# Kernel tuning notes

Hardware: AMD Instinct MI355X
Metric: run time of the kernel (lower is better)

The kernel has to match this reference:

```python
import jax, jax.numpy as jnp
import numpy as np

BOX = 120          # box_size
RES = 1.0          # resolution (also Gaussian sigma)
NTYPES = 11        # num_atom_types (hard-coded in module)
D = 2              # splat half-width in cells -> (2D+1)^3 = 125 voxels/atom
B = 4
NATOMS = 2200      # 200 atoms per type


def setup_inputs() -> dict:
    key = jax.random.key(0)
    # atoms uniformly inside the box interior so splats mostly land in-bounds
    coords = jax.random.uniform(key, (B, NATOMS * 3), dtype=jnp.float32,
                                minval=20.0, maxval=100.0)
    per_type = NATOMS // NTYPES
    num_atoms_of_type = jnp.full((B, NTYPES), per_type, dtype=jnp.int32)
    offsets = jnp.tile(jnp.arange(NTYPES, dtype=jnp.int32) * per_type, (B, 1))
    return {"input_coords": coords,
            "num_atoms_of_type": num_atoms_of_type,
            "offsets": offsets}


def _splat(coords, num_atoms_of_type, offsets):
    # coords: [B, N, 3]; per-atom Gaussian splat into typed volume
    Bn, N, _ = coords.shape
    atom_idx = jnp.arange(N)

    def per_batch_types(off, num):
        # atoms [off[t], off[t]+num[t]) belong to type t
        t = jnp.clip(jnp.searchsorted(off, atom_idx, side='right') - 1, 0, NTYPES - 1)
        valid = (atom_idx >= off[t]) & (atom_idx < off[t] + num[t])
        return t, valid

    types, valid = jax.vmap(per_batch_types)(offsets, num_atoms_of_type)  # [B,N]

    # (2D+1)^3 window of integer cell offsets
    w = jnp.arange(-D, D + 1)
    wx, wy, wz = jnp.meshgrid(w, w, w, indexing='ij')
    win = jnp.stack([wx.ravel(), wy.ravel(), wz.ravel()], axis=-1)  # [W,3]

    base = jnp.floor(coords / RES).astype(jnp.int32)                 # [B,N,3]
    cells = base[:, :, None, :] + win[None, None, :, :]              # [B,N,W,3]
    centers = cells.astype(coords.dtype) * RES                       # voxel coords
    r2 = jnp.sum((centers - coords[:, :, None, :]) ** 2, axis=-1)    # [B,N,W]
    vals = jnp.exp(-r2 / (RES * RES))                                # Gaussian density

    inb = jnp.all((cells >= 0) & (cells < BOX), axis=-1)             # [B,N,W]
    ok = inb & valid[:, :, None]
    flat = (types[:, :, None] * (BOX * BOX * BOX)
            + cells[..., 0] * (BOX * BOX) + cells[..., 1] * BOX + cells[..., 2])
    flat = jnp.where(ok, flat, NTYPES * BOX * BOX * BOX)  # out-of-range -> dropped
    vals = jnp.where(ok, vals, jnp.zeros_like(vals))

    def scatter(f, v):
        vol = jnp.zeros((NTYPES * BOX * BOX * BOX,), dtype=coords.dtype)
        return vol.at[f.ravel()].add(v.ravel(), mode='drop')

    vol = jax.vmap(scatter)(flat, vals)
    return vol.reshape(Bn, NTYPES, BOX, BOX, BOX)


def reference(input_coords, num_atoms_of_type, offsets):
    coords = input_coords.reshape(input_coords.shape[0], -1, 3)
    return _splat(coords, num_atoms_of_type, offsets)
```

## Files before the change

### kernel.cpp

```cpp
#include <hip/hip_runtime.h>


#define BOX    120
#define NTYPES 11
#define DHALF  2
#define BOX3   (BOX * BOX * BOX)

#define BINSZ   4
#define NBIN    30
#define NBIN2   (NBIN * NBIN)
#define CAP     64

__global__ void zero_counts_kernel(int* __restrict__ counts, int n) {
    int i = blockIdx.x * blockDim.x + threadIdx.x;
    if (i < n) counts[i] = 0;
}

__global__ void bin_kernel(const float* __restrict__ coords,
                           const int*  __restrict__ num_atoms_of_type,
                           const int*  __restrict__ offsets,
                           float4* __restrict__ bins,
                           int*    __restrict__ counts,
                           int batch, int natoms) {
    int gid = blockIdx.x * blockDim.x + threadIdx.x;
    if (gid >= batch * natoms) return;
    int b = gid / natoms;
    int i = gid - b * natoms;

    const float* c = coords + ((long long)b * natoms + i) * 3;
    float x = c[0], y = c[1], z = c[2];

    const int* off = offsets           + b * NTYPES;
    const int* num = num_atoms_of_type + b * NTYPES;

    int t = 0;
#pragma unroll
    for (int k = 1; k < NTYPES; ++k)
        if (off[k] <= i) t = k;
    if (!(i >= off[t] && i < off[t] + num[t])) return;

    int bx = (int)floorf(x);
    int by = (int)floorf(y);
    int bz = (int)floorf(z);
    if (bx < -DHALF || bx >= BOX + DHALF ||
        by < -DHALF || by >= BOX + DHALF ||
        bz < -DHALF || bz >= BOX + DHALF) return;

    int cbx = min(BOX - 1, max(0, bx)) / BINSZ;
    int cby = min(BOX - 1, max(0, by)) / BINSZ;
    int bin = b * NBIN2 + cbx * NBIN + cby;

    int slot = atomicAdd(&counts[bin], 1);
    if (slot < CAP)
        bins[(long long)bin * CAP + slot] =
            make_float4(x, y, z, __int_as_float(t));
}

__global__ void gather_kernel(const float4* __restrict__ bins,
                              const int*    __restrict__ counts,
                              float* __restrict__ out) {
    int bid = blockIdx.x;
    int y = bid % BOX; bid /= BOX;
    int x = bid % BOX; bid /= BOX;
    int b = bid;
    int z = threadIdx.x;
    bool zon = (z < BOX);

    float acc[NTYPES];
#pragma unroll
    for (int k = 0; k < NTYPES; ++k) acc[k] = 0.f;

    int bx0 = max(0, x - DHALF) / BINSZ;
    int bx1 = min(BOX - 1, x + DHALF) / BINSZ;
    int by0 = max(0, y - DHALF) / BINSZ;
    int by1 = min(BOX - 1, y + DHALF) / BINSZ;

    for (int cbx = bx0; cbx <= bx1; ++cbx) {
        for (int cby = by0; cby <= by1; ++cby) {
            int bin = b * NBIN2 + cbx * NBIN + cby;
            int cnt = min(counts[bin], CAP);
            const float4* lst = bins + (long long)bin * CAP;
            for (int j = 0; j < cnt; ++j) {
                float4 a = lst[j];
                int abx = (int)floorf(a.x);
                int aby = (int)floorf(a.y);
                int abz = (int)floorf(a.z);
                if (abs(x - abx) > DHALF || abs(y - aby) > DHALF) continue;
                bool hit = zon && (abs(z - abz) <= DHALF);
                float dx = (float)x - a.x;
                float dy = (float)y - a.y;
                float dz = (float)z - a.z;
                float r2 = dx * dx + dy * dy + dz * dz;
                float val = hit ? expf(-r2) : 0.f;
                int t = __float_as_int(a.w);
#pragma unroll
                for (int k = 0; k < NTYPES; ++k)
                    acc[k] += (t == k) ? val : 0.f;
            }
        }
    }

    if (zon) {
        int base = x * (BOX * BOX) + y * BOX + z;
#pragma unroll
        for (int k = 0; k < NTYPES; ++k)
            out[(long long)(b * NTYPES + k) * BOX3 + base] = acc[k];
    }
}

extern "C" void kernel_launch(void* const* d_in, const int* in_sizes, int n_in,
                              void* d_out, int out_size, void* d_ws, size_t ws_size,
                              hipStream_t stream) {
    const float* coords = (const float*)d_in[0];
    const int*   num    = (const int*)d_in[1];
    const int*   off    = (const int*)d_in[2];
    float*       out    = (float*)d_out;

    int batch  = in_sizes[1] / NTYPES;
    int natoms = in_sizes[0] / (3 * batch);

    int    nbins  = batch * NBIN2;
    int*   counts = (int*)d_ws;
    size_t bins_off = ((size_t)nbins * sizeof(int) + 15) & ~(size_t)15;
    float4* bins  = (float4*)((char*)d_ws + bins_off);

    zero_counts_kernel<<<(nbins + 255) / 256, 256, 0, stream>>>(counts, nbins);

    int natom_threads = batch * natoms;
    bin_kernel<<<(natom_threads + 255) / 256, 256, 0, stream>>>(
        coords, num, off, bins, counts, batch, natoms);

    gather_kernel<<<batch * BOX * BOX, 128, 0, stream>>>(bins, counts, out);
}
```

Measured before the change: 367.2 us.

## Tile gather over 8 y-rows with shared-memory atom lists sorted by type

Each gather block now handles one x-plane and 8 y-rows instead of a single (x,y) line. Threads cooperatively pull the candidate atoms from the bins into shared memory, precompute dx^2, and bucket them by type with a counting sort. Each thread then computes 4 consecutive z voxels with per-type accumulators and writes them as float4 stores. This removes redundant global bin reads and the per-atom 11-way type select, and vectorizes the output, at the cost of extra syncs, shared-memory atomics and a 512-atom shared capacity limit that could silently drop atoms in dense regions.

```diff
diff --git a/kernel.cpp b/kernel.cpp
--- a/kernel.cpp
+++ b/kernel.cpp
@@ -6,10 +6,14 @@
 #define DHALF  2
 #define BOX3   (BOX * BOX * BOX)
 
-#define BINSZ   4
-#define NBIN    30
-#define NBIN2   (NBIN * NBIN)
-#define CAP     64
+#define BINSZ  4
+#define NBIN   30
+#define NBIN2  (NBIN * NBIN)
+#define CAP    64
+
+#define YT     8
+#define NYT    (BOX / YT)
+#define SCAP   512
 
 __global__ void zero_counts_kernel(int* __restrict__ counts, int n) {
     int i = blockIdx.x * blockDim.x + threadIdx.x;
@@ -56,55 +60,121 @@
             make_float4(x, y, z, __int_as_float(t));
 }
 
-__global__ void gather_kernel(const float4* __restrict__ bins,
-                              const int*    __restrict__ counts,
-                              float* __restrict__ out) {
+__global__ __launch_bounds__(256)
+void gather_kernel(const float4* __restrict__ bins,
+                   const int*    __restrict__ counts,
+                   float* __restrict__ out) {
     int bid = blockIdx.x;
-    int y = bid % BOX; bid /= BOX;
-    int x = bid % BOX; bid /= BOX;
-    int b = bid;
-    int z = threadIdx.x;
-    bool zon = (z < BOX);
-
-    float acc[NTYPES];
-#pragma unroll
-    for (int k = 0; k < NTYPES; ++k) acc[k] = 0.f;
-
-    int bx0 = max(0, x - DHALF) / BINSZ;
-    int bx1 = min(BOX - 1, x + DHALF) / BINSZ;
-    int by0 = max(0, y - DHALF) / BINSZ;
-    int by1 = min(BOX - 1, y + DHALF) / BINSZ;
-
-    for (int cbx = bx0; cbx <= bx1; ++cbx) {
-        for (int cby = by0; cby <= by1; ++cby) {
+    int yt = bid % NYT; bid /= NYT;
+    int x  = bid % BOX; bid /= BOX;
+    int b  = bid;
+    int y0 = yt * YT;
+    float xf = (float)x;
+
+    __shared__ float4 raw[SCAP];
+    __shared__ float4 srt[SCAP];
+    __shared__ int cnt;
+    __shared__ int tcnt[NTYPES];
+    __shared__ int tstart[NTYPES + 1];
+    __shared__ int tidx[NTYPES];
+
+    if (threadIdx.x == 0) cnt = 0;
+    if (threadIdx.x < NTYPES) tcnt[threadIdx.x] = 0;
+    __syncthreads();
+
+    int bxlo = max(0, x - DHALF) / BINSZ;
+    int bxhi = min(BOX - 1, x + DHALF) / BINSZ;
+    int bylo = max(0, y0 - DHALF) / BINSZ;
+    int byhi = min(BOX - 1, y0 + YT - 1 + DHALF) / BINSZ;
+
+    for (int cbx = bxlo; cbx <= bxhi; ++cbx) {
+        for (int cby = bylo; cby <= byhi; ++cby) {
             int bin = b * NBIN2 + cbx * NBIN + cby;
-            int cnt = min(counts[bin], CAP);
+            int c = min(counts[bin], CAP);
             const float4* lst = bins + (long long)bin * CAP;
-            for (int j = 0; j < cnt; ++j) {
+            for (int j = threadIdx.x; j < c; j += blockDim.x) {
                 float4 a = lst[j];
-                int abx = (int)floorf(a.x);
-                int aby = (int)floorf(a.y);
-                int abz = (int)floorf(a.z);
-                if (abs(x - abx) > DHALF || abs(y - aby) > DHALF) continue;
-                bool hit = zon && (abs(z - abz) <= DHALF);
-                float dx = (float)x - a.x;
-                float dy = (float)y - a.y;
-                float dz = (float)z - a.z;
-                float r2 = dx * dx + dy * dy + dz * dz;
-                float val = hit ? expf(-r2) : 0.f;
-                int t = __float_as_int(a.w);
-#pragma unroll
-                for (int k = 0; k < NTYPES; ++k)
-                    acc[k] += (t == k) ? val : 0.f;
+                float abx = floorf(a.x);
+                float aby = floorf(a.y);
+                if (fabsf(xf - abx) <= (float)DHALF &&
+                    aby >= (float)(y0 - DHALF) &&
+                    aby <= (float)(y0 + YT - 1 + DHALF)) {
+                    int slot = atomicAdd(&cnt, 1);
+                    if (slot < SCAP) {
+                        int t = __float_as_int(a.w);
+                        atomicAdd(&tcnt[t], 1);
+                        float dx = xf - a.x;
+                        raw[slot] = make_float4(a.y, a.z, dx * dx, a.w);
+                    }
+                }
             }
         }
     }
-
-    if (zon) {
-        int base = x * (BOX * BOX) + y * BOX + z;
-#pragma unroll
-        for (int k = 0; k < NTYPES; ++k)
-            out[(long long)(b * NTYPES + k) * BOX3 + base] = acc[k];
+    __syncthreads();
+
+    int n = min(cnt, SCAP);
+    if (threadIdx.x == 0) {
+        int s = 0;
+#pragma unroll
+        for (int k = 0; k < NTYPES; ++k) {
+            tstart[k] = s; tidx[k] = s; s += tcnt[k];
+        }
+        tstart[NTYPES] = s;
+    }
+    __syncthreads();
+
+    for (int j = threadIdx.x; j < n; j += blockDim.x) {
+        float4 a = raw[j];
+        int t = __float_as_int(a.w);
+        int d = atomicAdd(&tidx[t], 1);
+        srt[d] = a;
+    }
+    __syncthreads();
+
+    int tt = threadIdx.x;
+    int yl = tt / 30;
+    int z4 = tt - yl * 30;
+    bool on = (tt < 240);
+    float yf  = (float)(y0 + yl);
+    float zf0 = (float)(z4 * 4);
+
+    float acc[NTYPES][4];
+#pragma unroll
+    for (int k = 0; k < NTYPES; ++k)
+#pragma unroll
+        for (int i = 0; i < 4; ++i) acc[k][i] = 0.f;
+
+#pragma unroll
+    for (int k = 0; k < NTYPES; ++k) {
+        int s = tstart[k], e = tstart[k + 1];
+        for (int j = s; j < e; ++j) {
+            float4 a = srt[j];
+            float ay = a.x, az = a.y, dx2 = a.z;
+            float aby = floorf(ay);
+            float abz = floorf(az);
+            bool yok = fabsf(yf - aby) <= (float)DHALF;
+            float dy  = yf - ay;
+            float c2  = fmaf(dy, dy, dx2);
+            float dz0  = zf0 - az;
+            float dzc0 = zf0 - abz;
+#pragma unroll
+            for (int i = 0; i < 4; ++i) {
+                float dz = dz0 + (float)i;
+                float r2 = fmaf(dz, dz, c2);
+                bool zok = fabsf(dzc0 + (float)i) <= (float)DHALF;
+                float v = (yok && zok) ? expf(-r2) : 0.f;
+                acc[k][i] += v;
+            }
+        }
+    }
+
+    if (on) {
+        int base = x * (BOX * BOX) + (y0 + yl) * BOX + z4 * 4;
+#pragma unroll
+        for (int k = 0; k < NTYPES; ++k) {
+            float4 v = make_float4(acc[k][0], acc[k][1], acc[k][2], acc[k][3]);
+            *reinterpret_cast<float4*>(&out[(long long)(b * NTYPES + k) * BOX3 + base]) = v;
+        }
     }
 }
 
@@ -130,5 +200,5 @@
     bin_kernel<<<(natom_threads + 255) / 256, 256, 0, stream>>>(
         coords, num, off, bins, counts, batch, natoms);
 
-    gather_kernel<<<batch * BOX * BOX, 128, 0, stream>>>(bins, counts, out);
-}
+    gather_kernel<<<batch * BOX * NYT, 256, 0, stream>>>(bins, counts, out);
+}
```

Result: faster. 324.1 us (-11.7%).
